# Kernel optimization log

Hardware: AMD Instinct MI355X
Metric: run time of the kernel (lower is better)

The kernel has to match this reference:

```python
import jax, jax.numpy as jnp
import numpy as np

N = 10000
IN_DIM = 256
HID = 256
HEADS = 8
NUM_CLASSES = 40
EPS = 1e-5
NEG_SLOPE = 0.2


def gat_conv(x, src, dst, W, a_src, a_dst, bias, concat):
    # x: [N, F_in]; W: [F_in, H*C]; a_src/a_dst: [H, C]
    n = x.shape[0]
    H, C = a_src.shape
    h = (x @ W).reshape(n, H, C)                       # [N,H,C]
    s_src = jnp.einsum('nhc,hc->nh', h, a_src)         # [N,H]
    s_dst = jnp.einsum('nhc,hc->nh', h, a_dst)         # [N,H]
    score = jax.nn.leaky_relu(s_src[src] + s_dst[dst], NEG_SLOPE)  # [E,H]
    m = jax.lax.stop_gradient(jax.ops.segment_max(score, dst, num_segments=n))
    e = jnp.exp(score - m[dst])                        # [E,H]
    denom = jax.ops.segment_sum(e, dst, num_segments=n)
    alpha = e / denom[dst]                             # per-dst edge softmax
    msg = h[src] * alpha[:, :, None]                   # [E,H,C]
    out = jax.ops.segment_sum(msg, dst, num_segments=n)  # [N,H,C]
    out = out.reshape(n, H * C) if concat else out.mean(axis=1)
    return out + bias


def batch_norm(x, gamma, beta):
    mu = x.mean(axis=0)
    var = x.var(axis=0)
    return gamma * (x - mu) * jax.lax.rsqrt(var + EPS) + beta


def setup_inputs() -> dict:
    key = jax.random.key(0)
    ks = jax.random.split(key, 16)
    C0 = HID // HEADS  # 32, concat layer
    x = jax.random.normal(ks[0], (N, IN_DIM), jnp.float32)
    edge_index = jax.random.randint(ks[1], (2, 160000), 0, N, jnp.int32)
    def lin(k, fi, fo):
        return jax.random.normal(k, (fi, fo), jnp.float32) / np.sqrt(fi)
    return {
        'x': x,
        'edge_index': edge_index,
        'W0': lin(ks[2], IN_DIM, HEADS * C0),
        'a_src0': jax.random.normal(ks[3], (HEADS, C0), jnp.float32) * 0.1,
        'a_dst0': jax.random.normal(ks[4], (HEADS, C0), jnp.float32) * 0.1,
        'b0': jnp.zeros((HID,), jnp.float32),
        'g0': jnp.ones((HID,), jnp.float32),
        'be0': jnp.zeros((HID,), jnp.float32),
        'W1': lin(ks[5], HID, HEADS * HID),
        'a_src1': jax.random.normal(ks[6], (HEADS, HID), jnp.float32) * 0.1,
        'a_dst1': jax.random.normal(ks[7], (HEADS, HID), jnp.float32) * 0.1,
        'b1': jnp.zeros((HID,), jnp.float32),
        'g1': jnp.ones((HID,), jnp.float32),
        'be1': jnp.zeros((HID,), jnp.float32),
        'Wc': lin(ks[8], HID, NUM_CLASSES),
        'bc': jnp.zeros((NUM_CLASSES,), jnp.float32),
    }


def reference(x, edge_index, W0, a_src0, a_dst0, b0, g0, be0,
              W1, a_src1, a_dst1, b1, g1, be1, Wc, bc):
    n = x.shape[0]
    loops = jnp.arange(n, dtype=edge_index.dtype)
    src = jnp.concatenate([edge_index[0], loops])  # add_self_loops=True
    dst = jnp.concatenate([edge_index[1], loops])

    # layer 0: concat=True -> [N, 256]
    h = gat_conv(x, src, dst, W0, a_src0, a_dst0, b0, concat=True)
    h = jax.nn.elu(batch_norm(h, g0, be0))
    # i==0: no residual; dropout is identity at eval

    # layer 1 (last): concat=False (mean over heads) -> [N, 256]
    h_in = h
    h = gat_conv(h, src, dst, W1, a_src1, a_dst1, b1, concat=False)
    h = jax.nn.elu(batch_norm(h, g1, be1)) + h_in  # residual for i>0

    return h @ Wc + bc  # logits [N, num_classes]
```

## Files before the change

### kernel.cpp

```cpp
#include <hip/hip_runtime.h>
#include <math.h>

#define NN 10000
#define HEADS 8
#define NCLS 40
#define CHK 64
#define LOG2E 1.4426950408889634f

typedef __attribute__((ext_vector_type(8))) short short8;
typedef __attribute__((ext_vector_type(8))) unsigned short ushort8v;
typedef __attribute__((ext_vector_type(4))) float floatx4;

static __device__ __forceinline__ short f2bf(float f) {
    unsigned u = __builtin_bit_cast(unsigned, f);
    unsigned r = (u + 0x7fff + ((u >> 16) & 1)) >> 16;
    return (short)r;
}
static __device__ __forceinline__ float bf2f(unsigned short u) {
    unsigned x = ((unsigned)u) << 16;
    return __builtin_bit_cast(float, x);
}
static __device__ __forceinline__ void gl2lds16(const void* g, void* l) {
    __builtin_amdgcn_global_load_lds(
        (const __attribute__((address_space(1))) unsigned int*)g,
        (__attribute__((address_space(3))) unsigned int*)l, 16, 0, 0);
}

__global__ __launch_bounds__(256) void gemm_bf16_w128(
    const short* __restrict__ A, const short* __restrict__ Bt,
    float* __restrict__ C, short* __restrict__ Cbf,
    float* __restrict__ stats,
    const float* __restrict__ asrc, const float* __restrict__ adst,
    float* __restrict__ s0,
    const int* __restrict__ esrc, const int* __restrict__ edst,
    int* __restrict__ cursor, int* __restrict__ elist, int E,
    int gemmBlocks, int gridY,
    int M, int Nn, int K, float alpha)
{
    if ((int)blockIdx.x >= gemmBlocks) {
        int e = ((int)blockIdx.x - gemmBlocks) * 256 + threadIdx.x;
        if (e < E) {
            int dn = edst[e];
            int pos = atomicAdd(&cursor[dn], 1);
            elist[pos] = esrc[e];
        }
        return;
    }
    __shared__ short As[64 * 64];
    __shared__ short Bs[128 * 64];
    const int tid = threadIdx.x;
    const int w = tid >> 6, L = tid & 63;
    const int quad = L >> 4, lr = L & 15;
    const int d = blockIdx.x;
    const int by = (d >> 4) * 8 + (d & 7);
    const int bx = (d >> 3) & 1;
    if (by >= gridY) return;
    const int col0 = bx * 128, row0 = by * 64;

    const int schunk = (L & 7) ^ (L >> 3);
    const int sarow = w * 16 + (L >> 3);
    int ga0 = row0 + sarow;     if (ga0 > M - 1) ga0 = M - 1;
    int ga1 = row0 + sarow + 8; if (ga1 > M - 1) ga1 = M - 1;
    const short* agp0 = A + (size_t)ga0 * K + schunk * 8;
    const short* agp1 = A + (size_t)ga1 * K + schunk * 8;
    short* alp0 = &As[w * 1024];
    short* alp1 = &As[w * 1024 + 512];
    const int sbrow = w * 32 + (L >> 3);
    int gb[4];
    #pragma unroll
    for (int c = 0; c < 4; c++) {
        gb[c] = col0 + sbrow + c * 8;
        if (gb[c] > Nn - 1) gb[c] = Nn - 1;
    }
    const short* bgp0 = Bt + (size_t)gb[0] * K + schunk * 8;
    const short* bgp1 = Bt + (size_t)gb[1] * K + schunk * 8;
    const short* bgp2 = Bt + (size_t)gb[2] * K + schunk * 8;
    const short* bgp3 = Bt + (size_t)gb[3] * K + schunk * 8;
    short* blp0 = &Bs[w * 2048];
    short* blp1 = &Bs[w * 2048 + 512];
    short* blp2 = &Bs[w * 2048 + 1024];
    short* blp3 = &Bs[w * 2048 + 1536];

    floatx4 acc[4][2];
    const floatx4 zf = {0.f, 0.f, 0.f, 0.f};
    #pragma unroll
    for (int i = 0; i < 4; i++)
        #pragma unroll
        for (int j = 0; j < 2; j++) acc[i][j] = zf;

    for (int k0 = 0; k0 < K; k0 += 64) {
        gl2lds16(agp0 + k0, alp0);
        gl2lds16(agp1 + k0, alp1);
        gl2lds16(bgp0 + k0, blp0);
        gl2lds16(bgp1 + k0, blp1);
        gl2lds16(bgp2 + k0, blp2);
        gl2lds16(bgp3 + k0, blp3);
        __syncthreads();
        #pragma unroll
        for (int ks = 0; ks < 2; ks++) {
            const int sl = ((ks * 4 + quad) ^ (lr & 7)) * 8;
            short8 bfr[2];
            #pragma unroll
            for (int j = 0; j < 2; j++)
                bfr[j] = *(const short8*)&Bs[(w * 32 + j * 16 + lr) * 64 + sl];
            #pragma unroll
            for (int i = 0; i < 4; i++) {
                short8 afr = *(const short8*)&As[(i * 16 + lr) * 64 + sl];
                #pragma unroll
                for (int j = 0; j < 2; j++)
                    acc[i][j] = __builtin_amdgcn_mfma_f32_16x16x32_bf16(afr, bfr[j], acc[i][j], 0, 0, 0);
            }
        }
        __syncthreads();
    }
    float s[2] = {0.f, 0.f}, s2[2] = {0.f, 0.f};
    #pragma unroll
    for (int j = 0; j < 2; j++) {
        int ccol = col0 + w * 32 + j * 16 + lr;
        if (ccol >= Nn) continue;
        #pragma unroll
        for (int i = 0; i < 4; i++) {
            #pragma unroll
            for (int r = 0; r < 4; r++) {
                int crow = row0 + i * 16 + quad * 4 + r;
                if (crow < M) {
                    float v = alpha * acc[i][j][r];
                    if (C)   C[(size_t)crow * Nn + ccol] = v;
                    if (Cbf) Cbf[(size_t)crow * Nn + ccol] = f2bf(v);
                    s[j] += v; s2[j] += v * v;
                }
            }
        }
    }
    if (stats) {
        #pragma unroll
        for (int j = 0; j < 2; j++) {
            s[j]  += __shfl_xor(s[j], 16, 64);  s[j]  += __shfl_xor(s[j], 32, 64);
            s2[j] += __shfl_xor(s2[j], 16, 64); s2[j] += __shfl_xor(s2[j], 32, 64);
        }
        if (L < 16) {
            #pragma unroll
            for (int j = 0; j < 2; j++) {
                int ccol = col0 + w * 32 + j * 16 + L;
                if (ccol < Nn) {
                    atomicAdd(&stats[ccol], s[j]);
                    atomicAdd(&stats[256 + ccol], s2[j]);
                }
            }
        }
    }
    if (s0) {
        const int head = bx * 4 + w;
        float as0 = asrc[col0 + w * 32 + lr];
        float as1 = asrc[col0 + w * 32 + 16 + lr];
        float ad0 = adst[col0 + w * 32 + lr];
        float ad1 = adst[col0 + w * 32 + 16 + lr];
        #pragma unroll
        for (int i = 0; i < 4; i++) {
            #pragma unroll
            for (int r = 0; r < 4; r++) {
                float ps = acc[i][0][r] * as0 + acc[i][1][r] * as1;
                float pd = acc[i][0][r] * ad0 + acc[i][1][r] * ad1;
                #pragma unroll
                for (int off = 1; off < 16; off <<= 1) {
                    ps += __shfl_xor(ps, off, 64);
                    pd += __shfl_xor(pd, off, 64);
                }
                if (lr == 0) {
                    int crow = row0 + i * 16 + quad * 4 + r;
                    if (crow < M) {
                        s0[crow * 16 + head] = alpha * ps;
                        s0[crow * 16 + 8 + head] = alpha * pd;
                    }
                }
            }
        }
    }
}

__global__ __launch_bounds__(256) void classifier_fused(
    const float* __restrict__ X, const float* __restrict__ stats,
    const float* __restrict__ g, const float* __restrict__ be,
    const unsigned short* __restrict__ resid,
    const short* __restrict__ Bt, float* __restrict__ C,
    const float* __restrict__ bias, int M, int Nn, int K)
{
    __shared__ short As[64 * 64];
    __shared__ short Bs[64 * 64];
    const int tid = threadIdx.x;
    const int w = tid >> 6, L = tid & 63;
    const int quad = L >> 4, lr = L & 15;
    const int row0 = blockIdx.x * 64;

    const int srow = w * 16 + (L >> 3);
    const int schunk = (L & 7) ^ (L >> 3);
    int ga0 = row0 + srow;     if (ga0 > M - 1)  ga0 = M - 1;
    int ga1 = row0 + srow + 8; if (ga1 > M - 1)  ga1 = M - 1;
    int gb0 = srow;     if (gb0 > Nn - 1) gb0 = Nn - 1;
    int gb1 = srow + 8; if (gb1 > Nn - 1) gb1 = Nn - 1;
    const float* xg0 = X + (size_t)ga0 * K + schunk * 8;
    const float* xg1 = X + (size_t)ga1 * K + schunk * 8;
    const unsigned short* rg0 = resid + (size_t)ga0 * K + schunk * 8;
    const unsigned short* rg1 = resid + (size_t)ga1 * K + schunk * 8;
    const short* bgp0 = Bt + (size_t)gb0 * K + schunk * 8;
    const short* bgp1 = Bt + (size_t)gb1 * K + schunk * 8;
    short* alw0 = &As[w * 1024 + L * 8];
    short* alw1 = &As[w * 1024 + 512 + L * 8];
    short* blp0 = &Bs[w * 1024];
    short* blp1 = &Bs[w * 1024 + 512];

    floatx4 acc[4];
    const floatx4 zf = {0.f, 0.f, 0.f, 0.f};
    #pragma unroll
    for (int i = 0; i < 4; i++) acc[i] = zf;
    const float invN = 1.0f / NN;

    for (int k0 = 0; k0 < K; k0 += 64) {
        gl2lds16(bgp0 + k0, blp0);
        gl2lds16(bgp1 + k0, blp1);
        const int c = schunk * 8 + k0;
        floatx4 mu_a = *(const floatx4*)(stats + c);
        floatx4 mu_b = *(const floatx4*)(stats + c + 4);
        floatx4 sq_a = *(const floatx4*)(stats + 256 + c);
        floatx4 sq_b = *(const floatx4*)(stats + 256 + c + 4);
        floatx4 g_a  = *(const floatx4*)(g + c);
        floatx4 g_b  = *(const floatx4*)(g + c + 4);
        floatx4 be_a = *(const floatx4*)(be + c);
        floatx4 be_b = *(const floatx4*)(be + c + 4);
        float scl[8], sh[8];
        #pragma unroll
        for (int q = 0; q < 8; q++) {
            float m  = (q < 4 ? mu_a[q & 3] : mu_b[q & 3]) * invN;
            float sq = (q < 4 ? sq_a[q & 3] : sq_b[q & 3]) * invN;
            float gv = (q < 4 ? g_a[q & 3]  : g_b[q & 3]);
            float bv = (q < 4 ? be_a[q & 3] : be_b[q & 3]);
            float rs = rsqrtf(sq - m * m + 1e-5f) * gv;
            scl[q] = rs; sh[q] = bv - m * rs;
        }
        {
            floatx4 xa = *(const floatx4*)(xg0 + k0);
            floatx4 xb2 = *(const floatx4*)(xg0 + k0 + 4);
            ushort8v rv = *(const ushort8v*)(rg0 + k0);
            short8 av;
            #pragma unroll
            for (int q = 0; q < 8; q++) {
                float v = (q < 4 ? xa[q & 3] : xb2[q & 3]) * scl[q] + sh[q];
                v = (v > 0.f) ? v : (expf(v) - 1.f);
                v += bf2f(rv[q]);
                av[q] = f2bf(v);
            }
            *(short8*)alw0 = av;
        }
        {
            floatx4 xa = *(const floatx4*)(xg1 + k0);
            floatx4 xb2 = *(const floatx4*)(xg1 + k0 + 4);
            ushort8v rv = *(const ushort8v*)(rg1 + k0);
            short8 av;
            #pragma unroll
            for (int q = 0; q < 8; q++) {
                float v = (q < 4 ? xa[q & 3] : xb2[q & 3]) * scl[q] + sh[q];
                v = (v > 0.f) ? v : (expf(v) - 1.f);
                v += bf2f(rv[q]);
                av[q] = f2bf(v);
            }
            *(short8*)alw1 = av;
        }
        __syncthreads();
        #pragma unroll
        for (int ks = 0; ks < 2; ks++) {
            const int sl = ((ks * 4 + quad) ^ (lr & 7)) * 8;
            short8 bfr = *(const short8*)&Bs[(w * 16 + lr) * 64 + sl];
            #pragma unroll
            for (int i = 0; i < 4; i++) {
                short8 afr = *(const short8*)&As[(i * 16 + lr) * 64 + sl];
                acc[i] = __builtin_amdgcn_mfma_f32_16x16x32_bf16(afr, bfr, acc[i], 0, 0, 0);
            }
        }
        __syncthreads();
    }
    const int ccol = w * 16 + lr;
    if (ccol < Nn) {
        float bv = bias ? bias[ccol] : 0.f;
        #pragma unroll
        for (int i = 0; i < 4; i++) {
            #pragma unroll
            for (int r = 0; r < 4; r++) {
                int crow = row0 + i * 16 + quad * 4 + r;
                if (crow < M) C[(size_t)crow * Nn + ccol] = acc[i][r] + bv;
            }
        }
    }
}

__global__ __launch_bounds__(1024) void scan_kernel(
    int* counts, int* offsets, int* cursor, int* elist, int n)
{
    const int P = (n + 1023) >> 10;
    __shared__ int wsum[16];
    int tid = threadIdx.x, lane = tid & 63, wid = tid >> 6;
    int base = tid * P;
    int local[16];
    int deg[16];
    int s = 0;
    for (int j = 0; j < P; j++) {
        int i = base + j;
        local[j] = s;
        deg[j] = (i < n) ? counts[i] + 1 : 0;
        s += deg[j];
    }
    int inc = s;
    #pragma unroll
    for (int off = 1; off < 64; off <<= 1) {
        int tv = __shfl_up(inc, off, 64);
        if (lane >= off) inc += tv;
    }
    if (lane == 63) wsum[wid] = inc;
    __syncthreads();
    if (tid < 16) {
        int v = wsum[tid];
        int winc = v;
        #pragma unroll
        for (int off = 1; off < 16; off <<= 1) {
            int tv = __shfl_up(winc, off, 16);
            if (tid >= off) winc += tv;
        }
        wsum[tid] = winc - v;
    }
    __syncthreads();
    int excl = inc - s + wsum[wid];
    for (int j = 0; j < P; j++) {
        int i = base + j;
        if (i < n) {
            int o = excl + local[j];
            counts[i] = deg[j];
            offsets[i] = o;
            elist[o] = i;
            cursor[i] = o + 1;
        }
    }
}

__global__ __launch_bounds__(256) void prep_count(
    const float* __restrict__ x, const float* __restrict__ W0,
    const float* __restrict__ W1, const float* __restrict__ a_src1,
    const float* __restrict__ a_dst1, const float* __restrict__ Wc,
    const int* __restrict__ edst, int E,
    short* __restrict__ xb, short* __restrict__ W0T, float* __restrict__ v1,
    short* __restrict__ W1pT, short* __restrict__ WcT, int* __restrict__ counts)
{
    __shared__ float tile[32][33];
    const int b = blockIdx.x, t = threadIdx.x;
    if (b < 2500) {
        int i = b * 256 + t;
        floatx4 v = ((const floatx4*)x)[i];
        short4 o = {f2bf(v[0]), f2bf(v[1]), f2bf(v[2]), f2bf(v[3])};
        ((short4*)xb)[i] = o;
    } else if (b < 2756) {
        int o = b - 2500;
        W0T[o * 256 + t] = f2bf(W0[t * 256 + o]);
    } else if (b < 2772) {
        int idx = (b - 2756) * 256 + t;
        int f = idx >> 4, j = idx & 15;
        int h = j & 7;
        const float* a = (j < 8) ? a_src1 : a_dst1;
        float s = 0.f;
        for (int c = 0; c < 256; c++)
            s += W1[f * 2048 + h * 256 + c] * a[h * 256 + c];
        v1[idx] = s;
    } else if (b < 3284) {
        int id = b - 2772;
        int h = id >> 6, f0 = ((id >> 3) & 7) * 32, c0 = (id & 7) * 32;
        int tx = t & 31, ty = t >> 5;
        for (int r = ty; r < 32; r += 8)
            tile[r][tx] = W1[(size_t)(f0 + r) * 2048 + h * 256 + c0 + tx];
        __syncthreads();
        for (int r = ty; r < 32; r += 8)
            W1pT[(size_t)(c0 + r) * 2048 + h * 256 + f0 + tx] = f2bf(tile[tx][r]);
    } else if (b < 3324) {
        int o = b - 3284;
        WcT[o * 256 + t] = f2bf(Wc[t * 40 + o]);
    } else {
        int e = (b - 3324) * 256 + t;
        if (e < E) atomicAdd(&counts[edst[e]], 1);
    }
}

__global__ __launch_bounds__(256) void agg0_fused(
    const unsigned short* __restrict__ h0b, const float* __restrict__ s0,
    const int* __restrict__ offsets, const int* __restrict__ counts,
    const int* __restrict__ elist, float* __restrict__ out)
{
    __shared__ float pw_s[4][CHK * 8];
    __shared__ int   sn_s[4][CHK];
    const int wid = threadIdx.x >> 6, L = threadIdx.x & 63;
    const int n = blockIdx.x * 4 + wid;
    float* pw = pw_s[wid];
    int*   sw = sn_s[wid];
    const int deg = counts[n], start = offsets[n];
    const int hL = L >> 3;

    floatx4 sda = *(const floatx4*)(s0 + n * 16 + 8);
    floatx4 sdb = *(const floatx4*)(s0 + n * 16 + 12);
    float sd[8] = {sda[0], sda[1], sda[2], sda[3], sdb[0], sdb[1], sdb[2], sdb[3]};
    float lp[8] = {0.f, 0.f, 0.f, 0.f, 0.f, 0.f, 0.f, 0.f};
    float a0 = 0.f, a1 = 0.f, a2 = 0.f, a3 = 0.f;

    for (int e0 = 0; e0 < deg; e0 += CHK) {
        int ch = deg - e0; if (ch > CHK) ch = CHK;
        if (L < ch) {
            int sn = elist[start + e0 + L];
            sw[L] = sn;
            floatx4 ssa = *(const floatx4*)(s0 + sn * 16);
            floatx4 ssb = *(const floatx4*)(s0 + sn * 16 + 4);
            float ss[8] = {ssa[0], ssa[1], ssa[2], ssa[3], ssb[0], ssb[1], ssb[2], ssb[3]};
            float p[8];
            #pragma unroll
            for (int h = 0; h < 8; h++) {
                float v = ss[h] + sd[h];
                v = (v > 0.f) ? v : 0.2f * v;
                p[h] = exp2f(v * LOG2E);
                lp[h] += p[h];
            }
            floatx4 p0 = {p[0], p[1], p[2], p[3]};
            floatx4 p1 = {p[4], p[5], p[6], p[7]};
            *(floatx4*)&pw[L * 8] = p0;
            *(floatx4*)&pw[L * 8 + 4] = p1;
        }
        for (int e = 0; e < ch; e++) {
            float wgt = pw[e * 8 + hL];
            ushort4 vv = *(const ushort4*)(h0b + (size_t)sw[e] * 256 + 4 * L);
            a0 += wgt * bf2f(vv.x);
            a1 += wgt * bf2f(vv.y);
            a2 += wgt * bf2f(vv.z);
            a3 += wgt * bf2f(vv.w);
        }
    }
    #pragma unroll
    for (int off = 1; off < 64; off <<= 1)
        #pragma unroll
        for (int h = 0; h < 8; h++)
            lp[h] += __shfl_xor(lp[h], off, 64);
    float inv = 1.f / lp[hL];
    floatx4 o = {a0 * inv, a1 * inv, a2 * inv, a3 * inv};
    *(floatx4*)(out + (size_t)n * 256 + 4 * L) = o;
}

__global__ __launch_bounds__(256) void agg1_full(
    const unsigned short* __restrict__ hb, const float* __restrict__ s1,
    const int* __restrict__ offsets, const int* __restrict__ counts,
    const int* __restrict__ elist, short* __restrict__ aggout)
{
    __shared__ float pw_s[4][CHK * 8];
    __shared__ int   sn_s[4][CHK];
    const int wid = threadIdx.x >> 6, L = threadIdx.x & 63;
    const int n = blockIdx.x * 4 + wid;
    float* pw = pw_s[wid];
    int*   sw = sn_s[wid];
    const int deg = counts[n], start = offsets[n];

    floatx4 sda = *(const floatx4*)(s1 + n * 16 + 8);
    floatx4 sdb = *(const floatx4*)(s1 + n * 16 + 12);
    float sd[8] = {sda[0], sda[1], sda[2], sda[3], sdb[0], sdb[1], sdb[2], sdb[3]};
    float lp[8] = {0.f, 0.f, 0.f, 0.f, 0.f, 0.f, 0.f, 0.f};
    float acc[8][4];
    #pragma unroll
    for (int h = 0; h < 8; h++)
        #pragma unroll
        for (int f = 0; f < 4; f++) acc[h][f] = 0.f;

    for (int e0 = 0; e0 < deg; e0 += CHK) {
        int ch = deg - e0; if (ch > CHK) ch = CHK;
        if (L < ch) {
            int sn = elist[start + e0 + L];
            sw[L] = sn;
            floatx4 ssa = *(const floatx4*)(s1 + sn * 16);
            floatx4 ssb = *(const floatx4*)(s1 + sn * 16 + 4);
            float ss[8] = {ssa[0], ssa[1], ssa[2], ssa[3], ssb[0], ssb[1], ssb[2], ssb[3]};
            float p[8];
            #pragma unroll
            for (int h = 0; h < 8; h++) {
                float v = ss[h] + sd[h];
                v = (v > 0.f) ? v : 0.2f * v;
                p[h] = exp2f(v * LOG2E);
                lp[h] += p[h];
            }
            floatx4 p0 = {p[0], p[1], p[2], p[3]};
            floatx4 p1 = {p[4], p[5], p[6], p[7]};
            *(floatx4*)&pw[L * 8] = p0;
            *(floatx4*)&pw[L * 8 + 4] = p1;
        }
        for (int e = 0; e < ch; e++) {
            floatx4 p0 = *(const floatx4*)&pw[e * 8];
            floatx4 p1 = *(const floatx4*)&pw[e * 8 + 4];
            ushort4 vv = *(const ushort4*)(hb + (size_t)sw[e] * 256 + 4 * L);
            float v0 = bf2f(vv.x), v1_ = bf2f(vv.y), v2 = bf2f(vv.z), v3 = bf2f(vv.w);
            #pragma unroll
            for (int h = 0; h < 4; h++) {
                acc[h][0] += p0[h] * v0;     acc[h][1] += p0[h] * v1_;
                acc[h][2] += p0[h] * v2;     acc[h][3] += p0[h] * v3;
                acc[h + 4][0] += p1[h] * v0; acc[h + 4][1] += p1[h] * v1_;
                acc[h + 4][2] += p1[h] * v2; acc[h + 4][3] += p1[h] * v3;
            }
        }
    }
    #pragma unroll
    for (int off = 1; off < 64; off <<= 1)
        #pragma unroll
        for (int h = 0; h < 8; h++)
            lp[h] += __shfl_xor(lp[h], off, 64);
    #pragma unroll
    for (int h = 0; h < 8; h++) {
        float inv = 1.f / lp[h];
        short4 o = {f2bf(acc[h][0] * inv), f2bf(acc[h][1] * inv),
                    f2bf(acc[h][2] * inv), f2bf(acc[h][3] * inv)};
        *(short4*)(aggout + (size_t)n * 2048 + h * 256 + 4 * L) = o;
    }
}

__global__ __launch_bounds__(256) void bn_stats_kernel(const float* __restrict__ x, float* stats, int n) {
    int t = threadIdx.x;
    int sub = t >> 6, c4 = (t & 63) * 4;
    floatx4 s = {0.f, 0.f, 0.f, 0.f}, s2 = {0.f, 0.f, 0.f, 0.f};
    for (int r = blockIdx.x * 4 + sub; r < n; r += gridDim.x * 4) {
        floatx4 v = *(const floatx4*)(x + (size_t)r * 256 + c4);
        s += v; s2 += v * v;
    }
    #pragma unroll
    for (int k = 0; k < 4; k++) {
        atomicAdd(&stats[c4 + k], s[k]);
        atomicAdd(&stats[256 + c4 + k], s2[k]);
    }
}

__global__ __launch_bounds__(256) void bnapply_score1(
    const float* __restrict__ xg, const float* __restrict__ stats,
    const float* __restrict__ g, const float* __restrict__ be,
    const float* __restrict__ v1, short* __restrict__ hactb, float* __restrict__ s1)
{
    __shared__ float row[256];
    __shared__ float part[16][17];
    const int n = blockIdx.x, t = threadIdx.x;
    const float invN = 1.0f / NN;
    float mu = stats[t] * invN;
    float var = stats[256 + t] * invN - mu * mu;
    float v = g[t] * (xg[(size_t)n * 256 + t] - mu) * rsqrtf(var + 1e-5f) + be[t];
    v = (v > 0.f) ? v : (expf(v) - 1.f);
    hactb[(size_t)n * 256 + t] = f2bf(v);
    row[t] = v;
    __syncthreads();
    int j = t & 15, f0 = t >> 4;
    float p = 0.f;
    #pragma unroll
    for (int k = 0; k < 16; k++)
        p += row[f0 * 16 + k] * v1[(f0 * 16 + k) * 16 + j];
    part[f0][j] = p;
    __syncthreads();
    if (t < 16) {
        float s = 0.f;
        #pragma unroll
        for (int k = 0; k < 16; k++) s += part[k][t];
        s1[n * 16 + t] = s;
    }
}

extern "C" void kernel_launch(void* const* d_in, const int* in_sizes, int n_in,
                              void* d_out, int out_size, void* d_ws, size_t ws_size,
                              hipStream_t stream) {
    const float* x      = (const float*)d_in[0];
    const int*   eidx   = (const int*)d_in[1];
    const float* W0     = (const float*)d_in[2];
    const float* a_src0 = (const float*)d_in[3];
    const float* a_dst0 = (const float*)d_in[4];
    const float* g0     = (const float*)d_in[6];
    const float* be0    = (const float*)d_in[7];
    const float* W1     = (const float*)d_in[8];
    const float* a_src1 = (const float*)d_in[9];
    const float* a_dst1 = (const float*)d_in[10];
    const float* g1     = (const float*)d_in[12];
    const float* be1    = (const float*)d_in[13];
    const float* Wc     = (const float*)d_in[14];
    const float* bc     = (const float*)d_in[15];
    float* out = (float*)d_out;

    const int E = in_sizes[1] / 2;
    const int* esrc = eidx;
    const int* edst = eidx + E;

    char* ws = (char*)d_ws;
    size_t off = 0;
    auto alloc = [&](size_t bytes) {
        void* p = ws + off;
        off += (bytes + 255) & ~(size_t)255;
        return p;
    };
    float* stats   = (float*)alloc(1024 * 4);
    int*   counts  = (int*)alloc(NN * 4);
    float* out1    = (float*)alloc((size_t)NN * 256 * 4);
    short* h0b     = (short*)alloc((size_t)NN * 256 * 2);
    short* xb      = (short*)alloc((size_t)NN * 256 * 2);
    float* s0      = (float*)alloc((size_t)NN * 16 * 4);
    float* s1      = (float*)alloc((size_t)NN * 16 * 4);
    float* v1      = (float*)alloc(4096 * 4);
    float* h_gat0  = (float*)alloc((size_t)NN * 256 * 4);
    short* hactb   = (short*)alloc((size_t)NN * 256 * 2);
    short* agg1bf  = (short*)alloc((size_t)NN * 2048 * 2);
    short* W0T     = (short*)alloc((size_t)256 * 256 * 2);
    short* W1pT    = (short*)alloc((size_t)256 * 2048 * 2);
    short* WcT     = (short*)alloc((size_t)64 * 256 * 2);
    int* offsets   = (int*)alloc((NN + 16) * 4);
    int* cursor    = (int*)alloc(NN * 4);
    int* elist     = (int*)alloc((size_t)(E + NN) * 4);

    float* stats0 = stats;
    float* stats1 = stats + 512;

    hipMemsetAsync(stats, 0, 1024 * 4 + NN * 4, stream);

    const int cntBlocks = (E + 255) / 256;
    prep_count<<<3324 + cntBlocks, 256, 0, stream>>>(
        x, W0, W1, a_src1, a_dst1, Wc, edst, E,
        xb, W0T, v1, W1pT, WcT, counts);

    scan_kernel<<<1, 1024, 0, stream>>>(counts, offsets, cursor, elist, NN);

    const int gy = (NN + 63) / 64;
    const int gB = 16 * ((gy + 7) / 8);

    gemm_bf16_w128<<<gB + cntBlocks, 256, 0, stream>>>(
        xb, W0T, nullptr, h0b, nullptr,
        a_src0, a_dst0, s0,
        esrc, edst, cursor, elist, E,
        gB, gy, NN, 256, 256, 1.0f);

    agg0_fused<<<NN / 4, 256, 0, stream>>>(
        (const unsigned short*)h0b, s0, offsets, counts, elist, h_gat0);
    bn_stats_kernel<<<64, 256, 0, stream>>>(h_gat0, stats0, NN);
    bnapply_score1<<<NN, 256, 0, stream>>>(h_gat0, stats0, g0, be0, v1, hactb, s1);

    agg1_full<<<NN / 4, 256, 0, stream>>>(
        (const unsigned short*)hactb, s1, offsets, counts, elist, agg1bf);
    gemm_bf16_w128<<<gB, 256, 0, stream>>>(
        agg1bf, W1pT, out1, nullptr, stats1,
        nullptr, nullptr, nullptr,
        nullptr, nullptr, nullptr, nullptr, 0,
        gB, gy, NN, 256, 2048, 0.125f);

    classifier_fused<<<gy, 256, 0, stream>>>(
        out1, stats1, g1, be1, (const unsigned short*)hactb,
        WcT, out, bc, NN, NCLS, 256);
}
```

Measured before the change: 285.0 us.

## Rebalance prep kernels, fold W1 prep into GEMM launch, unroll aggregation loops

```diff
diff --git a/kernel.cpp b/kernel.cpp
--- a/kernel.cpp
+++ b/kernel.cpp
@@ -33,22 +33,52 @@
     const float* __restrict__ asrc, const float* __restrict__ adst,
     float* __restrict__ s0,
     const int* __restrict__ esrc, const int* __restrict__ edst,
-    int* __restrict__ cursor, int* __restrict__ elist, int E,
+    int* __restrict__ cursor, int* __restrict__ elist, int E, int scatBlocks,
+    const float* __restrict__ W1, const float* __restrict__ a_src1,
+    const float* __restrict__ a_dst1, float* __restrict__ v1,
+    short* __restrict__ W1pT,
     int gemmBlocks, int gridY,
     int M, int Nn, int K, float alpha)
 {
-    if ((int)blockIdx.x >= gemmBlocks) {
-        int e = ((int)blockIdx.x - gemmBlocks) * 256 + threadIdx.x;
-        if (e < E) {
-            int dn = edst[e];
-            int pos = atomicAdd(&cursor[dn], 1);
-            elist[pos] = esrc[e];
-        }
-        return;
-    }
     __shared__ short As[64 * 64];
     __shared__ short Bs[128 * 64];
     const int tid = threadIdx.x;
+    if ((int)blockIdx.x >= gemmBlocks) {
+        int td = (int)blockIdx.x - gemmBlocks;
+        if (td < scatBlocks) {
+            int e = td * 256 + tid;
+            if (e < E) {
+                int dn = edst[e];
+                int pos = atomicAdd(&cursor[dn], 1);
+                elist[pos] = esrc[e];
+            }
+            return;
+        }
+        td -= scatBlocks;
+        if (td < 16) {
+            int idx = td * 256 + tid;
+            int f = idx >> 4, j = idx & 15;
+            int h = j & 7;
+            const float* a = (j < 8) ? a_src1 : a_dst1;
+            float s = 0.f;
+            for (int c = 0; c < 256; c++)
+                s += W1[f * 2048 + h * 256 + c] * a[h * 256 + c];
+            v1[idx] = s;
+            return;
+        }
+        td -= 16;
+        {
+            float (*tile)[33] = (float(*)[33])As;
+            int h = td >> 6, f0 = ((td >> 3) & 7) * 32, c0 = (td & 7) * 32;
+            int tx = tid & 31, ty = tid >> 5;
+            for (int r = ty; r < 32; r += 8)
+                tile[r][tx] = W1[(size_t)(f0 + r) * 2048 + h * 256 + c0 + tx];
+            __syncthreads();
+            for (int r = ty; r < 32; r += 8)
+                W1pT[(size_t)(c0 + r) * 2048 + h * 256 + f0 + tx] = f2bf(tile[tx][r]);
+            return;
+        }
+    }
     const int w = tid >> 6, L = tid & 63;
     const int quad = L >> 4, lr = L & 15;
     const int d = blockIdx.x;
@@ -292,96 +322,72 @@
     }
 }
 
-__global__ __launch_bounds__(1024) void scan_kernel(
-    int* counts, int* offsets, int* cursor, int* elist, int n)
+__global__ __launch_bounds__(256) void prep_a(
+    const float* __restrict__ x, const int* __restrict__ edst, int E,
+    short* __restrict__ xb, int* __restrict__ counts)
 {
-    const int P = (n + 1023) >> 10;
-    __shared__ int wsum[16];
-    int tid = threadIdx.x, lane = tid & 63, wid = tid >> 6;
-    int base = tid * P;
-    int local[16];
-    int deg[16];
-    int s = 0;
-    for (int j = 0; j < P; j++) {
-        int i = base + j;
-        local[j] = s;
-        deg[j] = (i < n) ? counts[i] + 1 : 0;
-        s += deg[j];
-    }
-    int inc = s;
-    #pragma unroll
-    for (int off = 1; off < 64; off <<= 1) {
-        int tv = __shfl_up(inc, off, 64);
-        if (lane >= off) inc += tv;
-    }
-    if (lane == 63) wsum[wid] = inc;
-    __syncthreads();
-    if (tid < 16) {
-        int v = wsum[tid];
-        int winc = v;
-        #pragma unroll
-        for (int off = 1; off < 16; off <<= 1) {
-            int tv = __shfl_up(winc, off, 16);
-            if (tid >= off) winc += tv;
-        }
-        wsum[tid] = winc - v;
-    }
-    __syncthreads();
-    int excl = inc - s + wsum[wid];
-    for (int j = 0; j < P; j++) {
-        int i = base + j;
-        if (i < n) {
-            int o = excl + local[j];
-            counts[i] = deg[j];
-            offsets[i] = o;
-            elist[o] = i;
-            cursor[i] = o + 1;
-        }
-    }
-}
-
-__global__ __launch_bounds__(256) void prep_count(
-    const float* __restrict__ x, const float* __restrict__ W0,
-    const float* __restrict__ W1, const float* __restrict__ a_src1,
-    const float* __restrict__ a_dst1, const float* __restrict__ Wc,
-    const int* __restrict__ edst, int E,
-    short* __restrict__ xb, short* __restrict__ W0T, float* __restrict__ v1,
-    short* __restrict__ W1pT, short* __restrict__ WcT, int* __restrict__ counts)
-{
-    __shared__ float tile[32][33];
     const int b = blockIdx.x, t = threadIdx.x;
     if (b < 2500) {
         int i = b * 256 + t;
         floatx4 v = ((const floatx4*)x)[i];
         short4 o = {f2bf(v[0]), f2bf(v[1]), f2bf(v[2]), f2bf(v[3])};
         ((short4*)xb)[i] = o;
-    } else if (b < 2756) {
-        int o = b - 2500;
-        W0T[o * 256 + t] = f2bf(W0[t * 256 + o]);
-    } else if (b < 2772) {
-        int idx = (b - 2756) * 256 + t;
-        int f = idx >> 4, j = idx & 15;
-        int h = j & 7;
-        const float* a = (j < 8) ? a_src1 : a_dst1;
-        float s = 0.f;
-        for (int c = 0; c < 256; c++)
-            s += W1[f * 2048 + h * 256 + c] * a[h * 256 + c];
-        v1[idx] = s;
-    } else if (b < 3284) {
-        int id = b - 2772;
-        int h = id >> 6, f0 = ((id >> 3) & 7) * 32, c0 = (id & 7) * 32;
-        int tx = t & 31, ty = t >> 5;
-        for (int r = ty; r < 32; r += 8)
-            tile[r][tx] = W1[(size_t)(f0 + r) * 2048 + h * 256 + c0 + tx];
-        __syncthreads();
-        for (int r = ty; r < 32; r += 8)
-            W1pT[(size_t)(c0 + r) * 2048 + h * 256 + f0 + tx] = f2bf(tile[tx][r]);
-    } else if (b < 3324) {
-        int o = b - 3284;
+    } else {
+        int e = (b - 2500) * 256 + t;
+        if (e < E) atomicAdd(&counts[edst[e]], 1);
+    }
+}
+
+__global__ __launch_bounds__(256) void prep_b(
+    const float* __restrict__ W0, const float* __restrict__ Wc,
+    short* __restrict__ W0T, short* __restrict__ WcT,
+    int* __restrict__ counts, int* __restrict__ offsets,
+    int* __restrict__ cursor, int* __restrict__ elist, int n)
+{
+    const int b = blockIdx.x, t = threadIdx.x;
+    if (b < 256) {
+        W0T[b * 256 + t] = f2bf(W0[t * 256 + b]);
+        return;
+    }
+    if (b < 296) {
+        int o = b - 256;
         WcT[o * 256 + t] = f2bf(Wc[t * 40 + o]);
-    } else {
-        int e = (b - 3324) * 256 + t;
-        if (e < E) atomicAdd(&counts[edst[e]], 1);
+        return;
+    }
+    __shared__ int wsum[4];
+    const int P = (n + 255) >> 8;
+    const int lane = t & 63, wid = t >> 6;
+    const int base = t * P;
+    int s = 0;
+    for (int j = 0; j < P; j++) {
+        int i = base + j;
+        if (i < n) s += counts[i] + 1;
+    }
+    int inc = s;
+    #pragma unroll
+    for (int off = 1; off < 64; off <<= 1) {
+        int tv = __shfl_up(inc, off, 64);
+        if (lane >= off) inc += tv;
+    }
+    if (lane == 63) wsum[wid] = inc;
+    __syncthreads();
+    int wo = 0;
+    #pragma unroll
+    for (int k2 = 0; k2 < 4; k2++) {
+        int v = wsum[k2];
+        if (k2 < wid) wo += v;
+    }
+    int run = wo + inc - s;
+    for (int j = 0; j < P; j++) {
+        int i = base + j;
+        if (i < n) {
+            int d2 = counts[i] + 1;
+            counts[i] = d2;
+            offsets[i] = run;
+            elist[run] = i;
+            cursor[i] = run + 1;
+            run += d2;
+        }
     }
 }
 
@@ -426,13 +432,22 @@
             *(floatx4*)&pw[L * 8] = p0;
             *(floatx4*)&pw[L * 8 + 4] = p1;
         }
-        for (int e = 0; e < ch; e++) {
-            float wgt = pw[e * 8 + hL];
-            ushort4 vv = *(const ushort4*)(h0b + (size_t)sw[e] * 256 + 4 * L);
-            a0 += wgt * bf2f(vv.x);
-            a1 += wgt * bf2f(vv.y);
-            a2 += wgt * bf2f(vv.z);
-            a3 += wgt * bf2f(vv.w);
+        int e = 0;
+        for (; e + 2 <= ch; e += 2) {
+            float wA = pw[e * 8 + hL];
+            float wB = pw[e * 8 + 8 + hL];
+            ushort4 vA = *(const ushort4*)(h0b + (size_t)sw[e] * 256 + 4 * L);
+            ushort4 vB = *(const ushort4*)(h0b + (size_t)sw[e + 1] * 256 + 4 * L);
+            a0 += wA * bf2f(vA.x); a1 += wA * bf2f(vA.y);
+            a2 += wA * bf2f(vA.z); a3 += wA * bf2f(vA.w);
+            a0 += wB * bf2f(vB.x); a1 += wB * bf2f(vB.y);
+            a2 += wB * bf2f(vB.z); a3 += wB * bf2f(vB.w);
+        }
+        if (e < ch) {
+            float wA = pw[e * 8 + hL];
+            ushort4 vA = *(const ushort4*)(h0b + (size_t)sw[e] * 256 + 4 * L);
+            a0 += wA * bf2f(vA.x); a1 += wA * bf2f(vA.y);
+            a2 += wA * bf2f(vA.z); a3 += wA * bf2f(vA.w);
         }
     }
     #pragma unroll
@@ -489,17 +504,42 @@
             *(floatx4*)&pw[L * 8] = p0;
             *(floatx4*)&pw[L * 8 + 4] = p1;
         }
-        for (int e = 0; e < ch; e++) {
-            floatx4 p0 = *(const floatx4*)&pw[e * 8];
-            floatx4 p1 = *(const floatx4*)&pw[e * 8 + 4];
-            ushort4 vv = *(const ushort4*)(hb + (size_t)sw[e] * 256 + 4 * L);
-            float v0 = bf2f(vv.x), v1_ = bf2f(vv.y), v2 = bf2f(vv.z), v3 = bf2f(vv.w);
+        int e = 0;
+        for (; e + 2 <= ch; e += 2) {
+            floatx4 p0A = *(const floatx4*)&pw[e * 8];
+            floatx4 p1A = *(const floatx4*)&pw[e * 8 + 4];
+            floatx4 p0B = *(const floatx4*)&pw[e * 8 + 8];
+            floatx4 p1B = *(const floatx4*)&pw[e * 8 + 12];
+            ushort4 vA = *(const ushort4*)(hb + (size_t)sw[e] * 256 + 4 * L);
+            ushort4 vB = *(const ushort4*)(hb + (size_t)sw[e + 1] * 256 + 4 * L);
+            float a0 = bf2f(vA.x), a1 = bf2f(vA.y), a2 = bf2f(vA.z), a3 = bf2f(vA.w);
+            float b0 = bf2f(vB.x), b1 = bf2f(vB.y), b2 = bf2f(vB.z), b3 = bf2f(vB.w);
             #pragma unroll
             for (int h = 0; h < 4; h++) {
-                acc[h][0] += p0[h] * v0;     acc[h][1] += p0[h] * v1_;
-                acc[h][2] += p0[h] * v2;     acc[h][3] += p0[h] * v3;
-                acc[h + 4][0] += p1[h] * v0; acc[h + 4][1] += p1[h] * v1_;
-                acc[h + 4][2] += p1[h] * v2; acc[h + 4][3] += p1[h] * v3;
+                acc[h][0] += p0A[h] * a0;     acc[h][1] += p0A[h] * a1;
+                acc[h][2] += p0A[h] * a2;     acc[h][3] += p0A[h] * a3;
+                acc[h + 4][0] += p1A[h] * a0; acc[h + 4][1] += p1A[h] * a1;
+                acc[h + 4][2] += p1A[h] * a2; acc[h + 4][3] += p1A[h] * a3;
+            }
+            #pragma unroll
+            for (int h = 0; h < 4; h++) {
+                acc[h][0] += p0B[h] * b0;     acc[h][1] += p0B[h] * b1;
+                acc[h][2] += p0B[h] * b2;     acc[h][3] += p0B[h] * b3;
+                acc[h + 4][0] += p1B[h] * b0; acc[h + 4][1] += p1B[h] * b1;
+                acc[h + 4][2] += p1B[h] * b2; acc[h + 4][3] += p1B[h] * b3;
+            }
+        }
+        if (e < ch) {
+            floatx4 p0A = *(const floatx4*)&pw[e * 8];
+            floatx4 p1A = *(const floatx4*)&pw[e * 8 + 4];
+            ushort4 vA = *(const ushort4*)(hb + (size_t)sw[e] * 256 + 4 * L);
+            float a0 = bf2f(vA.x), a1 = bf2f(vA.y), a2 = bf2f(vA.z), a3 = bf2f(vA.w);
+            #pragma unroll
+            for (int h = 0; h < 4; h++) {
+                acc[h][0] += p0A[h] * a0;     acc[h][1] += p0A[h] * a1;
+                acc[h][2] += p0A[h] * a2;     acc[h][3] += p0A[h] * a3;
+                acc[h + 4][0] += p1A[h] * a0; acc[h + 4][1] += p1A[h] * a1;
+                acc[h + 4][2] += p1A[h] * a2; acc[h + 4][3] += p1A[h] * a3;
             }
         }
     }
@@ -617,24 +657,24 @@
     hipMemsetAsync(stats, 0, 1024 * 4 + NN * 4, stream);
 
     const int cntBlocks = (E + 255) / 256;
-    prep_count<<<3324 + cntBlocks, 256, 0, stream>>>(
-        x, W0, W1, a_src1, a_dst1, Wc, edst, E,
-        xb, W0T, v1, W1pT, WcT, counts);
-
-    scan_kernel<<<1, 1024, 0, stream>>>(counts, offsets, cursor, elist, NN);
+
+    prep_a<<<2500 + cntBlocks, 256, 0, stream>>>(x, edst, E, xb, counts);
+
+    prep_b<<<297, 256, 0, stream>>>(W0, Wc, W0T, WcT, counts, offsets, cursor, elist, NN);
 
     const int gy = (NN + 63) / 64;
     const int gB = 16 * ((gy + 7) / 8);
 
-    gemm_bf16_w128<<<gB + cntBlocks, 256, 0, stream>>>(
+    gemm_bf16_w128<<<gB + cntBlocks + 528, 256, 0, stream>>>(
         xb, W0T, nullptr, h0b, nullptr,
         a_src0, a_dst0, s0,
-        esrc, edst, cursor, elist, E,
+        esrc, edst, cursor, elist, E, cntBlocks,
+        W1, a_src1, a_dst1, v1, W1pT,
         gB, gy, NN, 256, 256, 1.0f);
 
     agg0_fused<<<NN / 4, 256, 0, stream>>>(
         (const unsigned short*)h0b, s0, offsets, counts, elist, h_gat0);
-    bn_stats_kernel<<<64, 256, 0, stream>>>(h_gat0, stats0, NN);
+    bn_stats_kernel<<<256, 256, 0, stream>>>(h_gat0, stats0, NN);
     bnapply_score1<<<NN, 256, 0, stream>>>(h_gat0, stats0, g0, be0, v1, hactb, s1);
 
     agg1_full<<<NN / 4, 256, 0, stream>>>(
@@ -642,7 +682,8 @@
     gemm_bf16_w128<<<gB, 256, 0, stream>>>(
         agg1bf, W1pT, out1, nullptr, stats1,
         nullptr, nullptr, nullptr,
-        nullptr, nullptr, nullptr, nullptr, 0,
+        nullptr, nullptr, nullptr, nullptr, 0, 0,
+        nullptr, nullptr, nullptr, nullptr, nullptr,
         gB, gy, NN, 256, 2048, 0.125f);
 
     classifier_fused<<<gy, 256, 0, stream>>>(
```

New measurement: 371.2 us. +30.3%, slower.
